# Kernel optimization log

Measured on AMD Instinct MI355X. Metric: run time of the kernel, lower is better.

The kernel has to match this reference:

```python
import jax, jax.numpy as jnp
import numpy as np

B, S, D, H = 1, 2048, 2048, 32
HD = D // H
SCALE = float(HD) ** -0.5


def _rope(x, cos, sin):
    # x: (b, s, h, hd); interleaved-pair RoPE as in executorch apply_rotary_emb
    xr, xi = x[..., 0::2], x[..., 1::2]
    c = cos[None, :, None, :]
    s = sin[None, :, None, :]
    out = jnp.stack([xr * c - xi * s, xr * s + xi * c], axis=-1)
    return out.reshape(x.shape)


def setup_inputs() -> dict:
    key = jax.random.key(0)
    ks = jax.random.split(key, 8)
    hidden_states = jax.random.normal(ks[0], (B, S, D), jnp.float32)
    pos = jnp.arange(S, dtype=jnp.float32)
    inv = 1.0 / (10000.0 ** (jnp.arange(0, HD, 2, dtype=jnp.float32) / HD))
    ang = pos[:, None] * inv[None, :]  # (S, HD//2)
    freqs_cos = jnp.cos(ang)
    freqs_sin = jnp.sin(ang)
    causal = jnp.tril(jnp.ones((S, S), dtype=bool))
    attention_mask = jnp.where(causal, 0.0, -1e9).astype(jnp.float32)[None, None]
    k_cache = jax.random.normal(ks[1], (B, S, H, HD), jnp.float32)
    v_cache = jax.random.normal(ks[2], (B, S, H, HD), jnp.float32)
    k_mask = jnp.ones((B, S, 1, 1), jnp.float32)
    v_mask = jnp.ones((B, S, 1, 1), jnp.float32)
    # weights stored as (in, out); math-equivalent to torch Linear(out,in) @ W.T
    wq = jax.random.normal(ks[3], (D, D), jnp.float32) * 0.02
    wk = jax.random.normal(ks[4], (D, D), jnp.float32) * 0.02
    wv = jax.random.normal(ks[5], (D, D), jnp.float32) * 0.02
    wo = jax.random.normal(ks[6], (D, D), jnp.float32) * 0.02
    return {"hidden_states": hidden_states, "freqs_cos": freqs_cos,
            "freqs_sin": freqs_sin, "attention_mask": attention_mask,
            "k_cache": k_cache, "v_cache": v_cache,
            "k_mask": k_mask, "v_mask": v_mask,
            "wq": wq, "wk": wk, "wv": wv, "wo": wo}


def reference(hidden_states, freqs_cos, freqs_sin, attention_mask,
              k_cache, v_cache, k_mask, v_mask, wq, wk, wv, wo):
    b, s, _ = hidden_states.shape
    q = (hidden_states @ wq).reshape(b, s, H, HD)
    k = (hidden_states @ wk).reshape(b, s, H, HD)
    v = (hidden_states @ wv).reshape(b, s, H, HD)
    q = _rope(q, freqs_cos, freqs_sin)
    k = _rope(k, freqs_cos, freqs_sin)
    # mask-blend KV cache update
    k = k_cache * (1.0 - k_mask) + k * k_mask  # (b, S, H, HD)
    v = v_cache * (1.0 - v_mask) + v * v_mask
    qt = q.transpose(0, 2, 1, 3)  # (b, H, s, HD)
    kt = k.transpose(0, 2, 1, 3)
    vt = v.transpose(0, 2, 1, 3)
    attn = jnp.einsum('bhqd,bhkd->bhqk', qt, kt) * SCALE + attention_mask
    attn = jax.nn.softmax(attn, axis=-1)
    y = jnp.einsum('bhqk,bhkd->bhqd', attn, vt)  # (b, H, s, HD)
    # torch: y.transpose(0,1).contiguous().view(b, s, dim); valid since b == 1
    y = jnp.swapaxes(y, 0, 1).reshape(b, s, D)
    y = y @ wo
    return (y, k, v)
```

## Files before the change

kernel.cpp:

```cpp
#include <hip/hip_runtime.h>
#include <hip/hip_bf16.h>
#include <stdint.h>

typedef __bf16 bf16;
typedef __attribute__((ext_vector_type(8))) __bf16 bf16x8;
typedef __attribute__((ext_vector_type(4))) float f32x4;

#define SEQ 2048
#define DIM 2048
#define NHEAD 32
#define HD 64
#define ATT_SCALE 0.125f

__device__ __forceinline__ void gload16(void* lds, const void* g) {
  __builtin_amdgcn_global_load_lds(
      (const __attribute__((address_space(1))) unsigned int*)g,
      (__attribute__((address_space(3))) unsigned int*)lds, 16, 0, 0);
}

__device__ __forceinline__ f32x4 mfma16(bf16x8 a, bf16x8 b, f32x4 c) {
  return __builtin_amdgcn_mfma_f32_16x16x32_bf16(a, b, c, 0, 0, 0);
}

__global__ __launch_bounds__(256) void cvt_hs(const float* __restrict__ in,
                                              bf16* __restrict__ out) {
  size_t i = ((size_t)blockIdx.x * 256 + threadIdx.x) * 8;
  f32x4 a = *(const f32x4*)(in + i);
  f32x4 b = *(const f32x4*)(in + i + 4);
  bf16x8 o;
#pragma unroll
  for (int j = 0; j < 4; ++j) { o[j] = (bf16)a[j]; o[j + 4] = (bf16)b[j]; }
  *(bf16x8*)(out + i) = o;
}

__global__ __launch_bounds__(256) void wtrans(
    const float* __restrict__ w0, const float* __restrict__ w1,
    const float* __restrict__ w2, const float* __restrict__ w3,
    bf16* __restrict__ t0, bf16* __restrict__ t1,
    bf16* __restrict__ t2, bf16* __restrict__ t3) {
  const float* wsrc[4] = {w0, w1, w2, w3};
  bf16* wdst[4] = {t0, t1, t2, t3};
  const float* w = wsrc[blockIdx.z];
  bf16* wT = wdst[blockIdx.z];
  __shared__ alignas(16) bf16 tile[64][72];
  int t = threadIdx.x;
  int n0 = blockIdx.x * 64, k0 = blockIdx.y * 64;
#pragma unroll
  for (int i = 0; i < 4; ++i) {
    int r = (t >> 4) + 16 * i;
    int c = (t & 15) * 4;
    f32x4 v = *(const f32x4*)(w + (size_t)(k0 + r) * DIM + n0 + c);
#pragma unroll
    for (int j = 0; j < 4; ++j) tile[r][c + j] = (bf16)v[j];
  }
  __syncthreads();
#pragma unroll
  for (int i = 0; i < 2; ++i) {
    int n = (t >> 3) + 32 * i;
    int kb = (t & 7) * 8;
    bf16x8 o;
#pragma unroll
    for (int j = 0; j < 8; ++j) o[j] = tile[kb + j][n];
    *(bf16x8*)(wT + (size_t)(n0 + n) * DIM + k0 + kb) = o;
  }
}

template <typename OutT>
__global__ __launch_bounds__(256) void gemm128(
    const bf16* __restrict__ A,
    const bf16* __restrict__ B0, const bf16* __restrict__ B1, const bf16* __restrict__ B2,
    OutT* __restrict__ C0, OutT* __restrict__ C1, OutT* __restrict__ C2,
    int M, int N, int K) {
  const bf16* Bt; OutT* C;
  if (blockIdx.z == 0)      { Bt = B0; C = C0; }
  else if (blockIdx.z == 1) { Bt = B1; C = C1; }
  else                      { Bt = B2; C = C2; }
  __shared__ alignas(16) bf16 As[128][64];
  __shared__ alignas(16) bf16 Bs[128][64];
  int tid = threadIdx.x, lane = tid & 63, w = tid >> 6;
  int wr = w >> 1, wc = w & 1;
  size_t mBase = (size_t)blockIdx.y * 128, nBase = (size_t)blockIdx.x * 128;
  f32x4 acc[4][4] = {};
  int r0 = tid >> 3, sl = tid & 7;
  int lr = lane & 15, hi = lane >> 4, sw = lr & 7;
  for (int kt = 0; kt < K; kt += 64) {
#pragma unroll
    for (int i = 0; i < 4; ++i) {
      int row = r0 + 32 * i;
      int kc = sl ^ (row & 7);
      gload16(&As[row][sl * 8], A + (mBase + row) * K + kt + kc * 8);
      gload16(&Bs[row][sl * 8], Bt + (nBase + row) * K + kt + kc * 8);
    }
    __syncthreads();
#pragma unroll
    for (int kk = 0; kk < 2; ++kk) {
      int cb = kk * 4 + hi;
      bf16x8 a[4], b[4];
#pragma unroll
      for (int m = 0; m < 4; ++m)
        a[m] = *(const bf16x8*)&As[wr * 64 + m * 16 + lr][(cb ^ sw) * 8];
#pragma unroll
      for (int n = 0; n < 4; ++n)
        b[n] = *(const bf16x8*)&Bs[wc * 64 + n * 16 + lr][(cb ^ sw) * 8];
#pragma unroll
      for (int m = 0; m < 4; ++m)
#pragma unroll
        for (int n = 0; n < 4; ++n)
          acc[m][n] = mfma16(a[m], b[n], acc[m][n]);
    }
    __syncthreads();
  }
#pragma unroll
  for (int m = 0; m < 4; ++m)
#pragma unroll
    for (int n = 0; n < 4; ++n)
#pragma unroll
      for (int j = 0; j < 4; ++j) {
        size_t row = mBase + wr * 64 + m * 16 + hi * 4 + j;
        size_t col = nBase + wc * 64 + n * 16 + lr;
        C[row * N + col] = (OutT)acc[m][n][j];
      }
}

__global__ __launch_bounds__(256) void ropeqk(
    const bf16* __restrict__ qraw, const bf16* __restrict__ kraw,
    const float* __restrict__ fc, const float* __restrict__ fs,
    const float* __restrict__ kcache, const float* __restrict__ kmask,
    float* __restrict__ kout, bf16* __restrict__ qb, bf16* __restrict__ kb) {
  int s = blockIdx.x;
  float km = kmask[s];
  float omk = 1.0f - km;
  for (int p = threadIdx.x; p < DIM / 2; p += 256) {
    int h = p >> 5, i = p & 31;
    float c = fc[s * 32 + i], sn = fs[s * 32 + i];
    size_t src = (size_t)s * DIM + h * 64 + 2 * i;
    float xr = (float)qraw[src], xi = (float)qraw[src + 1];
    float q0v = xr * c - xi * sn, q1v = xr * sn + xi * c;
    size_t dsth = (size_t)h * SEQ * HD + (size_t)s * HD + 2 * i;
    qb[dsth] = (bf16)q0v; qb[dsth + 1] = (bf16)q1v;
    xr = (float)kraw[src]; xi = (float)kraw[src + 1];
    float k0v = xr * c - xi * sn, k1v = xr * sn + xi * c;
    float b0 = kcache[src] * omk + k0v * km;
    float b1 = kcache[src + 1] * omk + k1v * km;
    kout[src] = b0; kout[src + 1] = b1;
    kb[dsth] = (bf16)b0; kb[dsth + 1] = (bf16)b1;
  }
}

__global__ __launch_bounds__(256) void vprep(
    const bf16* __restrict__ vraw, const float* __restrict__ vcache,
    const float* __restrict__ vmask, float* __restrict__ vout,
    bf16* __restrict__ vtb) {
  int h = blockIdx.y;
  int s0 = blockIdx.x * 64;
  __shared__ alignas(16) bf16 tile[64][72];
  int t = threadIdx.x;
#pragma unroll
  for (int i = 0; i < 4; ++i) {
    int r = (t >> 4) + 16 * i;
    int c = (t & 15) * 4;
    int s = s0 + r;
    float vm = vmask[s], om = 1.0f - vm;
    size_t src = (size_t)s * DIM + h * 64 + c;
    f32x4 vc = *(const f32x4*)(vcache + src);
    f32x4 o;
#pragma unroll
    for (int j = 0; j < 4; ++j) {
      float val = vc[j] * om + (float)vraw[src + j] * vm;
      o[j] = val;
      tile[r][c + j] = (bf16)val;
    }
    *(f32x4*)(vout + src) = o;
  }
  __syncthreads();
#pragma unroll
  for (int i = 0; i < 2; ++i) {
    int hd = (t >> 3) + 32 * i;
    int cb = (t & 7) * 8;
    bf16x8 o;
#pragma unroll
    for (int j = 0; j < 8; ++j) o[j] = tile[cb + j][hd];
    *(bf16x8*)(vtb + (size_t)h * HD * SEQ + (size_t)hd * SEQ + s0 + cb) = o;
  }
}

__global__ __launch_bounds__(256) void attn_fwd(
    const bf16* __restrict__ qb, const bf16* __restrict__ kb,
    const bf16* __restrict__ vtb, bf16* __restrict__ ob) {
  int h = blockIdx.y;
  int qt = (h & 1) ? (31 - (int)blockIdx.x) : (int)blockIdx.x;
  int q0 = qt * 64;
  __shared__ alignas(16) bf16 Ks[2][64][64];
  __shared__ alignas(16) bf16 Vs[2][64][64];
  __shared__ alignas(16) bf16 Ps[4][16][64];
  int tid = threadIdx.x, lane = tid & 63, w = tid >> 6;
  const bf16* qh = qb + (size_t)h * SEQ * HD;
  const bf16* kh = kb + (size_t)h * SEQ * HD;
  const bf16* vh = vtb + (size_t)h * HD * SEQ;
  int lr = lane & 15, hi = lane >> 4, sw = lr & 7;
  int qrow = q0 + w * 16 + lr;
  bf16x8 qf[2];
#pragma unroll
  for (int kk = 0; kk < 2; ++kk)
    qf[kk] = *(const bf16x8*)(qh + (size_t)qrow * HD + kk * 32 + hi * 8);
  f32x4 ot[4] = {};
  float mrun = -3e38f, lrun = 0.f;
  int nt = qt + 1;
  int r0 = tid >> 3, sl = tid & 7;
  char* PsW = (char*)&Ps[w][0][0];

  auto STAGE = [&](int t, int b) {
    int kv0 = t * 64;
#pragma unroll
    for (int i = 0; i < 2; ++i) {
      int row = r0 + 32 * i;
      int kc = sl ^ (row & 7);
      gload16(&Ks[b][row][sl * 8], kh + (size_t)(kv0 + row) * HD + kc * 8);
      gload16(&Vs[b][row][sl * 8], vh + (size_t)row * SEQ + kv0 + kc * 8);
    }
  };

  STAGE(0, 0);
  int buf = 0;
  for (int t = 0; t < nt; ++t) {
    __syncthreads();
    if (t + 1 < nt) STAGE(t + 1, buf ^ 1);
    int kv0 = t * 64;
    f32x4 st[4] = {};
    __builtin_amdgcn_s_setprio(1);
#pragma unroll
    for (int kk = 0; kk < 2; ++kk) {
      int cb = kk * 4 + hi;
#pragma unroll
      for (int n = 0; n < 4; ++n) {
        bf16x8 kf = *(const bf16x8*)&Ks[buf][n * 16 + lr][(cb ^ sw) * 8];
        st[n] = mfma16(kf, qf[kk], st[n]);
      }
    }
    __builtin_amdgcn_s_setprio(0);
    float tmax = -3e38f;
    if (t == nt - 1) {
#pragma unroll
      for (int n = 0; n < 4; ++n)
#pragma unroll
        for (int j = 0; j < 4; ++j) {
          int key = kv0 + n * 16 + hi * 4 + j;
          float v = (key <= qrow) ? st[n][j] * ATT_SCALE : -1e30f;
          st[n][j] = v;
          tmax = fmaxf(tmax, v);
        }
    } else {
#pragma unroll
      for (int n = 0; n < 4; ++n)
#pragma unroll
        for (int j = 0; j < 4; ++j) {
          float v = st[n][j] * ATT_SCALE;
          st[n][j] = v;
          tmax = fmaxf(tmax, v);
        }
    }
    tmax = fmaxf(tmax, __shfl_xor(tmax, 16));
    tmax = fmaxf(tmax, __shfl_xor(tmax, 32));
    float mnew = fmaxf(mrun, tmax);
    float psum = 0.f;
    if (__all(tmax <= mrun)) {
#pragma unroll
      for (int n = 0; n < 4; ++n)
#pragma unroll
        for (int j = 0; j < 4; ++j) {
          float p = __expf(st[n][j] - mrun);
          st[n][j] = p;
          psum += p;
        }
      psum += __shfl_xor(psum, 16);
      psum += __shfl_xor(psum, 32);
      lrun += psum;
    } else {
      float alpha = __expf(mrun - mnew);
#pragma unroll
      for (int n = 0; n < 4; ++n)
#pragma unroll
        for (int j = 0; j < 4; ++j) {
          float p = __expf(st[n][j] - mnew);
          st[n][j] = p;
          psum += p;
        }
      psum += __shfl_xor(psum, 16);
      psum += __shfl_xor(psum, 32);
      lrun = lrun * alpha + psum;
      mrun = mnew;
#pragma unroll
      for (int nd = 0; nd < 4; ++nd)
#pragma unroll
        for (int j = 0; j < 4; ++j) ot[nd][j] *= alpha;
    }
#pragma unroll
    for (int n = 0; n < 4; ++n) {
      union { bf16 b[4]; uint2 u; } pk;
#pragma unroll
      for (int j = 0; j < 4; ++j) pk.b[j] = (bf16)st[n][j];
      int keyc = n * 2 + (hi >> 1);
      *(uint2*)(PsW + lr * 128 + ((keyc ^ sw) * 16) + (hi & 1) * 8) = pk.u;
    }
    __builtin_amdgcn_s_setprio(1);
#pragma unroll
    for (int kk = 0; kk < 2; ++kk) {
      int cb = kk * 4 + hi;
      bf16x8 pf = *(const bf16x8*)(PsW + lr * 128 + ((cb ^ sw) * 16));
#pragma unroll
      for (int nd = 0; nd < 4; ++nd) {
        bf16x8 vf = *(const bf16x8*)&Vs[buf][nd * 16 + lr][(cb ^ sw) * 8];
        ot[nd] = mfma16(vf, pf, ot[nd]);
      }
    }
    __builtin_amdgcn_s_setprio(0);
    buf ^= 1;
  }
  float rinv = 1.0f / lrun;
  bf16* orow = ob + ((size_t)h * SEQ + qrow) * HD;
#pragma unroll
  for (int nd = 0; nd < 4; ++nd) {
    union { bf16 b[4]; uint2 u; } o;
#pragma unroll
    for (int j = 0; j < 4; ++j) o.b[j] = (bf16)(ot[nd][j] * rinv);
    *(uint2*)(orow + nd * 16 + hi * 4) = o.u;
  }
}

extern "C" void kernel_launch(void* const* d_in, const int* in_sizes, int n_in,
                              void* d_out, int out_size, void* d_ws, size_t ws_size,
                              hipStream_t stream) {
  const float* hs     = (const float*)d_in[0];
  const float* fc     = (const float*)d_in[1];
  const float* fs     = (const float*)d_in[2];
  const float* kcache = (const float*)d_in[4];
  const float* vcache = (const float*)d_in[5];
  const float* kmask  = (const float*)d_in[6];
  const float* vmask  = (const float*)d_in[7];
  const float* wq     = (const float*)d_in[8];
  const float* wk     = (const float*)d_in[9];
  const float* wv     = (const float*)d_in[10];
  const float* wo     = (const float*)d_in[11];

  float* y    = (float*)d_out;
  float* kout = y + (size_t)SEQ * DIM;
  float* vout = y + 2 * (size_t)SEQ * DIM;

  char* ws = (char*)d_ws;
  const size_t MB8 = (size_t)SEQ * DIM * sizeof(bf16);
  bf16* wqT  = (bf16*)(ws + 0 * MB8);
  bf16* wkT  = (bf16*)(ws + 1 * MB8);
  bf16* wvT  = (bf16*)(ws + 2 * MB8);
  bf16* woT  = (bf16*)(ws + 3 * MB8);
  bf16* hsb  = (bf16*)(ws + 4 * MB8);
  bf16* qraw = (bf16*)(ws + 5 * MB8);
  bf16* kraw = (bf16*)(ws + 6 * MB8);
  bf16* vraw = (bf16*)(ws + 7 * MB8);
  bf16* qb   = (bf16*)(ws + 8 * MB8);
  bf16* kb   = (bf16*)(ws + 9 * MB8);
  bf16* vtb  = (bf16*)(ws + 10 * MB8);
  bf16* ob   = hsb;

  cvt_hs<<<dim3(SEQ * DIM / 2048), dim3(256), 0, stream>>>(hs, hsb);
  wtrans<<<dim3(32, 32, 4), dim3(256), 0, stream>>>(wq, wk, wv, wo, wqT, wkT, wvT, woT);
  gemm128<bf16><<<dim3(16, 16, 3), dim3(256), 0, stream>>>(
      hsb, wqT, wkT, wvT, qraw, kraw, vraw, SEQ, DIM, DIM);
  ropeqk<<<dim3(SEQ), dim3(256), 0, stream>>>(qraw, kraw, fc, fs, kcache, kmask, kout, qb, kb);
  vprep<<<dim3(32, 32), dim3(256), 0, stream>>>(vraw, vcache, vmask, vout, vtb);
  attn_fwd<<<dim3(32, NHEAD), dim3(256), 0, stream>>>(qb, kb, vtb, ob);
  gemm128<float><<<dim3(16, 16, 1), dim3(256), 0, stream>>>(
      ob, woT, woT, woT, y, y, y, SEQ, DIM, DIM);
}
```

Before: 228.4 us.

## Load K/V fragments directly from global memory in attention, use exp2 softmax

The attention kernel stops staging K and V tiles through double-buffered LDS with a block-wide barrier. Each wave now loads its MFMA K and V fragments straight from global memory into registers. The scale is folded with log2(e) so exp2f can replace __expf. The grid becomes 1-D, ordered longest-first across heads, with a launch-bounds occupancy hint of 4. This removes LDS traffic and __syncthreads, but the four waves now fetch the same K/V redundantly from L2, and register pressure rises.

```diff
diff --git a/kernel.cpp b/kernel.cpp
--- a/kernel.cpp
+++ b/kernel.cpp
@@ -11,6 +11,7 @@
 #define NHEAD 32
 #define HD 64
 #define ATT_SCALE 0.125f
+#define SCALE_L2E 0.1803368801111244f
 
 __device__ __forceinline__ void gload16(void* lds, const void* g) {
   __builtin_amdgcn_global_load_lds(
@@ -184,14 +185,13 @@
   }
 }
 
-__global__ __launch_bounds__(256) void attn_fwd(
+__global__ __launch_bounds__(256, 4) void attn_fwd(
     const bf16* __restrict__ qb, const bf16* __restrict__ kb,
     const bf16* __restrict__ vtb, bf16* __restrict__ ob) {
-  int h = blockIdx.y;
-  int qt = (h & 1) ? (31 - (int)blockIdx.x) : (int)blockIdx.x;
+  int bid = blockIdx.x;
+  int h = bid & 31;
+  int qt = 31 - (bid >> 5);
   int q0 = qt * 64;
-  __shared__ alignas(16) bf16 Ks[2][64][64];
-  __shared__ alignas(16) bf16 Vs[2][64][64];
   __shared__ alignas(16) bf16 Ps[4][16][64];
   int tid = threadIdx.x, lane = tid & 63, w = tid >> 6;
   const bf16* qh = qb + (size_t)h * SEQ * HD;
@@ -206,38 +206,32 @@
   f32x4 ot[4] = {};
   float mrun = -3e38f, lrun = 0.f;
   int nt = qt + 1;
-  int r0 = tid >> 3, sl = tid & 7;
   char* PsW = (char*)&Ps[w][0][0];
 
-  auto STAGE = [&](int t, int b) {
+  for (int t = 0; t < nt; ++t) {
     int kv0 = t * 64;
-#pragma unroll
-    for (int i = 0; i < 2; ++i) {
-      int row = r0 + 32 * i;
-      int kc = sl ^ (row & 7);
-      gload16(&Ks[b][row][sl * 8], kh + (size_t)(kv0 + row) * HD + kc * 8);
-      gload16(&Vs[b][row][sl * 8], vh + (size_t)row * SEQ + kv0 + kc * 8);
-    }
-  };
-
-  STAGE(0, 0);
-  int buf = 0;
-  for (int t = 0; t < nt; ++t) {
-    __syncthreads();
-    if (t + 1 < nt) STAGE(t + 1, buf ^ 1);
-    int kv0 = t * 64;
+    bf16x8 kf[2][4];
+#pragma unroll
+    for (int kk = 0; kk < 2; ++kk)
+#pragma unroll
+      for (int n = 0; n < 4; ++n)
+        kf[kk][n] = *(const bf16x8*)(kh + (size_t)(kv0 + n * 16 + lr) * HD +
+                                     (kk * 4 + hi) * 8);
     f32x4 st[4] = {};
     __builtin_amdgcn_s_setprio(1);
 #pragma unroll
-    for (int kk = 0; kk < 2; ++kk) {
-      int cb = kk * 4 + hi;
-#pragma unroll
-      for (int n = 0; n < 4; ++n) {
-        bf16x8 kf = *(const bf16x8*)&Ks[buf][n * 16 + lr][(cb ^ sw) * 8];
-        st[n] = mfma16(kf, qf[kk], st[n]);
-      }
-    }
+    for (int kk = 0; kk < 2; ++kk)
+#pragma unroll
+      for (int n = 0; n < 4; ++n)
+        st[n] = mfma16(kf[kk][n], qf[kk], st[n]);
     __builtin_amdgcn_s_setprio(0);
+    bf16x8 vf[2][4];
+#pragma unroll
+    for (int kk = 0; kk < 2; ++kk)
+#pragma unroll
+      for (int nd = 0; nd < 4; ++nd)
+        vf[kk][nd] = *(const bf16x8*)(vh + (size_t)(nd * 16 + lr) * SEQ + kv0 +
+                                      (kk * 4 + hi) * 8);
     float tmax = -3e38f;
     if (t == nt - 1) {
 #pragma unroll
@@ -245,7 +239,7 @@
 #pragma unroll
         for (int j = 0; j < 4; ++j) {
           int key = kv0 + n * 16 + hi * 4 + j;
-          float v = (key <= qrow) ? st[n][j] * ATT_SCALE : -1e30f;
+          float v = (key <= qrow) ? st[n][j] * SCALE_L2E : -3e38f;
           st[n][j] = v;
           tmax = fmaxf(tmax, v);
         }
@@ -254,7 +248,7 @@
       for (int n = 0; n < 4; ++n)
 #pragma unroll
         for (int j = 0; j < 4; ++j) {
-          float v = st[n][j] * ATT_SCALE;
+          float v = st[n][j] * SCALE_L2E;
           st[n][j] = v;
           tmax = fmaxf(tmax, v);
         }
@@ -268,7 +262,7 @@
       for (int n = 0; n < 4; ++n)
 #pragma unroll
         for (int j = 0; j < 4; ++j) {
-          float p = __expf(st[n][j] - mrun);
+          float p = exp2f(st[n][j] - mrun);
           st[n][j] = p;
           psum += p;
         }
@@ -276,12 +270,12 @@
       psum += __shfl_xor(psum, 32);
       lrun += psum;
     } else {
-      float alpha = __expf(mrun - mnew);
+      float alpha = exp2f(mrun - mnew);
 #pragma unroll
       for (int n = 0; n < 4; ++n)
 #pragma unroll
         for (int j = 0; j < 4; ++j) {
-          float p = __expf(st[n][j] - mnew);
+          float p = exp2f(st[n][j] - mnew);
           st[n][j] = p;
           psum += p;
         }
@@ -308,13 +302,10 @@
       int cb = kk * 4 + hi;
       bf16x8 pf = *(const bf16x8*)(PsW + lr * 128 + ((cb ^ sw) * 16));
 #pragma unroll
-      for (int nd = 0; nd < 4; ++nd) {
-        bf16x8 vf = *(const bf16x8*)&Vs[buf][nd * 16 + lr][(cb ^ sw) * 8];
-        ot[nd] = mfma16(vf, pf, ot[nd]);
-      }
+      for (int nd = 0; nd < 4; ++nd)
+        ot[nd] = mfma16(vf[kk][nd], pf, ot[nd]);
     }
     __builtin_amdgcn_s_setprio(0);
-    buf ^= 1;
   }
   float rinv = 1.0f / lrun;
   bf16* orow = ob + ((size_t)h * SEQ + qrow) * HD;
@@ -367,7 +358,7 @@
       hsb, wqT, wkT, wvT, qraw, kraw, vraw, SEQ, DIM, DIM);
   ropeqk<<<dim3(SEQ), dim3(256), 0, stream>>>(qraw, kraw, fc, fs, kcache, kmask, kout, qb, kb);
   vprep<<<dim3(32, 32), dim3(256), 0, stream>>>(vraw, vcache, vmask, vout, vtb);
-  attn_fwd<<<dim3(32, NHEAD), dim3(256), 0, stream>>>(qb, kb, vtb, ob);
+  attn_fwd<<<dim3(1024), dim3(256), 0, stream>>>(qb, kb, vtb, ob);
   gemm128<float><<<dim3(16, 16, 1), dim3(256), 0, stream>>>(
       ob, woT, woT, woT, y, y, y, SEQ, DIM, DIM);
 }
```

New measurement: 303.4 us. +32.8%, slower.
